# Kernel optimization log

Hardware: AMD Instinct MI355X
Metric: run time of the kernel (lower is better)

The kernel has to match this reference:

```python
import jax, jax.numpy as jnp
import numpy as np

DIM = 192
HEADS = 4
B, H, W = 4, 128, 128


def _dwconv3(x, w):
    # depthwise 3x3, padding=1: w has shape [C, 1, 3, 3], groups = C
    return jax.lax.conv_general_dilated(
        x, w, window_strides=(1, 1), padding='SAME',
        feature_group_count=x.shape[1],
        dimension_numbers=('NCHW', 'OIHW', 'NCHW'))


def _conv1x1(x, w):
    # w: [O, C] (squeezed 1x1 kernel), bias=False
    return jnp.einsum('bchw,oc->bohw', x, w)


def _l2norm(t):
    # torch F.normalize(dim=-1), eps=1e-12
    n = jnp.sqrt(jnp.sum(t * t, axis=-1, keepdims=True))
    return t / jnp.maximum(n, 1e-12)


def setup_inputs() -> dict:
    key = jax.random.key(0)
    ks = jax.random.split(key, 12)
    s = 0.05
    return {
        'x': jax.random.normal(ks[0], (B, DIM, H, W), jnp.float32),
        'x_hidden': jax.random.normal(ks[1], (B, DIM, H, W), jnp.float32),
        'qkv_w': jax.random.normal(ks[2], (3 * DIM, DIM), jnp.float32) * s,
        'qkv_dw_w': jax.random.normal(ks[3], (3 * DIM, 1, 3, 3), jnp.float32) * s,
        'q_mut_w': jax.random.normal(ks[4], (DIM, DIM), jnp.float32) * s,
        'q_mut_dw_w': jax.random.normal(ks[5], (DIM, 1, 3, 3), jnp.float32) * s,
        'kv_mut_w': jax.random.normal(ks[6], (2 * DIM, DIM), jnp.float32) * s,
        'kv_mut_dw_w': jax.random.normal(ks[7], (2 * DIM, 1, 3, 3), jnp.float32) * s,
        'proj_w': jax.random.normal(ks[8], (DIM, 2 * DIM), jnp.float32) * s,
        'temperature': jnp.ones((HEADS, 1, 1), jnp.float32),
        'temperature_mut': jnp.ones((HEADS, 1, 1), jnp.float32),
    }


def reference(x, x_hidden, qkv_w, qkv_dw_w, q_mut_w, q_mut_dw_w,
              kv_mut_w, kv_mut_dw_w, proj_w, temperature, temperature_mut):
    b, c, h, w = x.shape
    heads = HEADS

    qkv = _dwconv3(_conv1x1(x, qkv_w), qkv_dw_w)
    q, k, v = jnp.split(qkv, 3, axis=1)
    q_mut = _dwconv3(_conv1x1(x, q_mut_w), q_mut_dw_w)
    kv_mut = _dwconv3(_conv1x1(x_hidden, kv_mut_w), kv_mut_dw_w)
    k_mut, v_mut = jnp.split(kv_mut, 2, axis=1)

    def rs(t):  # b (head c') h w -> b head c' (h w)
        return t.reshape(b, heads, c // heads, h * w)

    q, k, v = rs(q), rs(k), rs(v)
    q_mut, k_mut, v_mut = rs(q_mut), rs(k_mut), rs(v_mut)

    q, k = _l2norm(q), _l2norm(k)
    q_mut, k_mut = _l2norm(q_mut), _l2norm(k_mut)

    # channel-wise (transposed) attention: [b, head, c', c']
    attn = jax.nn.softmax(
        jnp.einsum('bhcn,bhdn->bhcd', q, k) * temperature, axis=-1)
    cross = jax.nn.softmax(
        jnp.einsum('bhcn,bhdn->bhcd', q_mut, k_mut) * temperature_mut, axis=-1)

    out = jnp.einsum('bhcd,bhdn->bhcn', attn, v).reshape(b, c, h, w)
    out_mut = jnp.einsum('bhcd,bhdn->bhcn', cross, v_mut).reshape(b, c, h, w)

    return _conv1x1(jnp.concatenate((out, out_mut), axis=1), proj_w)
```

## Files before the change

kernel.cpp:

```cpp
#include <hip/hip_runtime.h>
#include <hip/hip_bf16.h>

typedef __hip_bfloat16 bf16;
using short8  = __attribute__((ext_vector_type(8))) short;
using float4_ = __attribute__((ext_vector_type(4))) float;

#define B_    4
#define C_    192
#define NN    16384
#define HEADS 4
#define CHD   48
#define TOT   1152

__device__ __forceinline__ float b2f(bf16 v) { return __bfloat162float(v); }
__device__ __forceinline__ float s2f(short s) {
    return __uint_as_float(((unsigned)(unsigned short)s) << 16);
}

__global__ __launch_bounds__(256) void kprep_w(
    const float* __restrict__ qkv_w, const float* __restrict__ qm_w,
    const float* __restrict__ kvm_w, bf16* __restrict__ Wb)
{
    int i = blockIdx.x * 256 + threadIdx.x;
    if (i >= TOT * C_) return;
    int r = i / C_, c = i % C_;
    float v = (r < 576) ? qkv_w[r * C_ + c]
            : (r < 768) ? qm_w[(r - 576) * C_ + c]
                        : kvm_w[(r - 768) * C_ + c];
    Wb[i] = __float2bfloat16(v);
}

__global__ __launch_bounds__(256) void kprep_x(
    const float* __restrict__ x, const float* __restrict__ xh,
    int b, bf16* __restrict__ Xt)
{
    const int src = blockIdx.z;
    const float* in = (src == 0 ? x : xh) + (size_t)b * C_ * NN;
    bf16* outp = Xt + (size_t)src * NN * C_;
    const int n0 = blockIdx.x * 32, c0 = blockIdx.y * 32;
    __shared__ float t[32][33];
    const int tid = threadIdx.x;
    const int ln = tid & 31, lc = tid >> 5;
    #pragma unroll
    for (int it = 0; it < 4; ++it)
        t[lc + it * 8][ln] = in[(size_t)(c0 + lc + it * 8) * NN + n0 + ln];
    __syncthreads();
    const int lc2 = tid & 31, ln2 = tid >> 5;
    #pragma unroll
    for (int it = 0; it < 4; ++it)
        outp[(size_t)(n0 + ln2 + it * 8) * C_ + c0 + lc2] =
            __float2bfloat16(t[lc2][ln2 + it * 8]);
}

__global__ __launch_bounds__(256) void kgemm(
    const bf16* __restrict__ Wb, const bf16* __restrict__ Xt,
    bf16* __restrict__ Y)
{
    const int nt0 = blockIdx.x * 128;
    const int mt0 = blockIdx.y * 64;
    const int tid = threadIdx.x;
    const bf16* Xs = Xt + (mt0 >= 768 ? (size_t)NN * C_ : 0);

    __shared__ short sA[64][72];
    __shared__ short sB[128][72];

    const int wave = tid >> 6, lane = tid & 63;
    const int mw = (wave & 1) * 32, nw = (wave >> 1) * 64;
    const int lm = lane & 15, lq = lane >> 4;

    float4_ acc[2][4];
    #pragma unroll
    for (int i = 0; i < 2; ++i)
        #pragma unroll
        for (int j = 0; j < 4; ++j)
            acc[i][j] = (float4_){0.f, 0.f, 0.f, 0.f};

    for (int kc = 0; kc < 192; kc += 64) {
        __syncthreads();
        {
            int r = tid >> 3, c8 = (tid & 7) * 8;
            #pragma unroll
            for (int it = 0; it < 2; ++it, r += 32)
                *(short8*)&sA[r][c8] =
                    *(const short8*)&Wb[(size_t)(mt0 + r) * C_ + kc + c8];
        }
        {
            int r = tid >> 3, c8 = (tid & 7) * 8;
            #pragma unroll
            for (int it = 0; it < 4; ++it, r += 32)
                *(short8*)&sB[r][c8] =
                    *(const short8*)&Xs[(size_t)(nt0 + r) * C_ + kc + c8];
        }
        __syncthreads();
        #pragma unroll
        for (int kk = 0; kk < 64; kk += 32) {
            short8 af[2], bfr[4];
            const int ko = kk + lq * 8;
            #pragma unroll
            for (int i = 0; i < 2; ++i)
                af[i] = *(const short8*)&sA[mw + i * 16 + lm][ko];
            #pragma unroll
            for (int j = 0; j < 4; ++j)
                bfr[j] = *(const short8*)&sB[nw + j * 16 + lm][ko];
            #pragma unroll
            for (int i = 0; i < 2; ++i)
                #pragma unroll
                for (int j = 0; j < 4; ++j)
                    acc[i][j] = __builtin_amdgcn_mfma_f32_16x16x32_bf16(
                        af[i], bfr[j], acc[i][j], 0, 0, 0);
        }
    }
    #pragma unroll
    for (int i = 0; i < 2; ++i)
        #pragma unroll
        for (int j = 0; j < 4; ++j) {
            const int n = nt0 + nw + j * 16 + lm;
            #pragma unroll
            for (int r = 0; r < 4; ++r) {
                const int m = mt0 + mw + i * 16 + lq * 4 + r;
                Y[(size_t)m * NN + n] = __float2bfloat16(acc[i][j][r]);
            }
        }
}

__device__ __forceinline__ void kdw_load_row(
    float* r, const bf16* __restrict__ Yc, int row, int x0, int lane)
{
    float f[8];
    if (row >= 0 && row <= 127) {
        short8 v = *(const short8*)(Yc + row * 128 + x0);
        #pragma unroll
        for (int i = 0; i < 8; ++i) f[i] = s2f(v[i]);
    } else {
        #pragma unroll
        for (int i = 0; i < 8; ++i) f[i] = 0.f;
    }
    const float lf = __shfl(f[7], lane - 1);
    const float rf = __shfl(f[0], lane + 1);
    r[0] = (x0 > 0)   ? lf : 0.f;
    r[9] = (x0 < 120) ? rf : 0.f;
    #pragma unroll
    for (int i = 0; i < 8; ++i) r[i + 1] = f[i];
}

__global__ __launch_bounds__(256) void kdw(
    const bf16* __restrict__ Y,
    const float* __restrict__ qkv_dw, const float* __restrict__ qm_dw,
    const float* __restrict__ kvm_dw, int b, bf16* __restrict__ QT,
    float* __restrict__ nrmsq)
{
    const int ch  = blockIdx.x;
    const int tid = threadIdx.x;
    const int tx = tid & 15, ty = tid >> 4;
    const int lane = tid & 63;
    const int x0 = tx * 8;
    const int y0 = blockIdx.y * 64 + ty * 4;

    const float* dwp = (ch < 576) ? qkv_dw + (size_t)ch * 9
                     : (ch < 768) ? qm_dw + (size_t)(ch - 576) * 9
                                  : kvm_dw + (size_t)(ch - 768) * 9;
    float w[9];
    #pragma unroll
    for (int i = 0; i < 9; ++i) w[i] = dwp[i];

    const bf16* Yc = Y + (size_t)ch * NN;
    bf16* qout = QT + ((size_t)b * TOT + ch) * NN;

    float r0[10], r1[10], r2[10];
    kdw_load_row(r0, Yc, y0 - 1, x0, lane);
    kdw_load_row(r1, Yc, y0,     x0, lane);

    float ssq = 0.f;
    #pragma unroll
    for (int yy = 0; yy < 4; ++yy) {
        kdw_load_row(r2, Yc, y0 + yy + 1, x0, lane);
        short8 sv;
        #pragma unroll
        for (int xx = 0; xx < 8; ++xx) {
            float s = w[0] * r0[xx] + w[1] * r0[xx + 1] + w[2] * r0[xx + 2]
                    + w[3] * r1[xx] + w[4] * r1[xx + 1] + w[5] * r1[xx + 2]
                    + w[6] * r2[xx] + w[7] * r2[xx + 1] + w[8] * r2[xx + 2];
            ssq += s * s;
            bf16 h = __float2bfloat16(s);
            sv[xx] = *reinterpret_cast<short*>(&h);
        }
        *(short8*)&qout[(size_t)(y0 + yy) * 128 + x0] = sv;
        #pragma unroll
        for (int i = 0; i < 10; ++i) { r0[i] = r1[i]; r1[i] = r2[i]; }
    }

    int cls = -1, ci = 0;
    if (ch < 192)                    { cls = 0; ci = ch; }
    else if (ch < 384)               { cls = 1; ci = ch - 192; }
    else if (ch >= 576 && ch < 768)  { cls = 2; ci = ch - 576; }
    else if (ch >= 768 && ch < 960)  { cls = 3; ci = ch - 768; }
    if (cls >= 0) {
        #pragma unroll
        for (int off = 32; off > 0; off >>= 1) ssq += __shfl_down(ssq, off);
        __shared__ float red[4];
        if ((tid & 63) == 0) red[tid >> 6] = ssq;
        __syncthreads();
        if (tid == 0)
            atomicAdd(&nrmsq[(b * 4 + cls) * 192 + ci],
                      red[0] + red[1] + red[2] + red[3]);
    }
}

__global__ __launch_bounds__(256) void k3_mfma(
    const bf16* __restrict__ QT, float* __restrict__ Gpart)
{
    const int chunk = blockIdx.x;
    const int t = blockIdx.y >> 2, h = blockIdx.y & 3;
    const int b = blockIdx.z;
    const int qch = (t == 0 ? 0 : 576) + h * CHD;
    const int kch = (t == 0 ? 192 : 768) + h * CHD;
    const bf16* qp = QT + ((size_t)b * TOT + qch) * NN;
    const bf16* kp = QT + ((size_t)b * TOT + kch) * NN;

    const int tid = threadIdx.x;
    const int wave = tid >> 6, lane = tid & 63;
    const int lm = lane & 15, lq = lane >> 4;
    const int n0 = chunk * 512 + wave * 128;

    float4_ acc[3][3];
    #pragma unroll
    for (int i = 0; i < 3; ++i)
        #pragma unroll
        for (int j = 0; j < 3; ++j)
            acc[i][j] = (float4_){0.f, 0.f, 0.f, 0.f};

    #pragma unroll
    for (int kk = 0; kk < 128; kk += 32) {
        short8 af[3], bfr[3];
        const int ko = n0 + kk + lq * 8;
        #pragma unroll
        for (int i = 0; i < 3; ++i)
            af[i] = *(const short8*)&qp[(size_t)(i * 16 + lm) * NN + ko];
        #pragma unroll
        for (int j = 0; j < 3; ++j)
            bfr[j] = *(const short8*)&kp[(size_t)(j * 16 + lm) * NN + ko];
        #pragma unroll
        for (int i = 0; i < 3; ++i)
            #pragma unroll
            for (int j = 0; j < 3; ++j)
                acc[i][j] = __builtin_amdgcn_mfma_f32_16x16x32_bf16(
                    af[i], bfr[j], acc[i][j], 0, 0, 0);
    }

    __shared__ float sW[4][48 * 49];
    #pragma unroll
    for (int i = 0; i < 3; ++i)
        #pragma unroll
        for (int j = 0; j < 3; ++j)
            #pragma unroll
            for (int r = 0; r < 4; ++r)
                sW[wave][(i * 16 + lq * 4 + r) * 49 + j * 16 + lm] = acc[i][j][r];
    __syncthreads();

    const int gidx = ((t * 4 + b) * 4 + h);
    float* Gp = Gpart + ((size_t)gidx * 32 + chunk) * 2304;
    for (int idx = tid; idx < 2304; idx += 256) {
        const int c = idx / 48, d = idx % 48;
        Gp[idx] = sW[0][c * 49 + d] + sW[1][c * 49 + d]
                + sW[2][c * 49 + d] + sW[3][c * 49 + d];
    }
}

__global__ __launch_bounds__(256) void kred(
    const float* __restrict__ Gpart, float* __restrict__ G)
{
    const int idx = blockIdx.x * 256 + threadIdx.x;
    if (idx >= 32 * 2304) return;
    const int g = idx / 2304, i = idx % 2304;
    const float* p = Gpart + (size_t)g * 32 * 2304 + i;
    float s = 0.f;
    #pragma unroll
    for (int ch = 0; ch < 32; ++ch) s += p[(size_t)ch * 2304];
    G[(size_t)g * 2304 + i] = s;
}

__global__ __launch_bounds__(256) void k4a_softmax(
    const float* __restrict__ G, const float* __restrict__ nrmsq,
    const float* __restrict__ tq, const float* __restrict__ tm,
    float* __restrict__ P)
{
    const int gidx = blockIdx.x;
    const int h = gidx & 3, tb = gidx >> 2;
    const int b = tb & 3, t = tb >> 2;
    const float* Gp = G + (size_t)gidx * 2304;
    float* Pp = P + (size_t)gidx * 2304;

    const int tid = threadIdx.x;
    const int wave = tid >> 6, lane = tid & 63;
    const int clsq = (t == 0) ? 0 : 2, clsk = (t == 0) ? 1 : 3;
    const float tmp = (t == 0 ? tq[h] : tm[h]);

    float nk = 1.f;
    if (lane < 48)
        nk = fmaxf(sqrtf(fmaxf(nrmsq[(b * 4 + clsk) * 192 + h * 48 + lane], 0.f)),
                   1e-12f);
    const float sk = tmp / nk;

    const int c0 = blockIdx.y * 12 + wave * 3;
    #pragma unroll
    for (int cc = 0; cc < 3; ++cc) {
        const int c = c0 + cc;
        const float nq =
            fmaxf(sqrtf(fmaxf(nrmsq[(b * 4 + clsq) * 192 + h * 48 + c], 0.f)),
                  1e-12f);
        float L = -1e30f;
        if (lane < 48) L = Gp[c * 48 + lane] * sk / nq;
        float mx = L;
        #pragma unroll
        for (int off = 32; off > 0; off >>= 1)
            mx = fmaxf(mx, __shfl_xor(mx, off));
        float e = (lane < 48) ? expf(L - mx) : 0.f;
        float sum = e;
        #pragma unroll
        for (int off = 32; off > 0; off >>= 1)
            sum += __shfl_xor(sum, off);
        if (lane < 48) Pp[c * 48 + lane] = e / sum;
    }
}

__global__ __launch_bounds__(256) void k4b_fold(
    const float* __restrict__ P, const float* __restrict__ proj_w,
    bf16* __restrict__ Mb)
{
    const int gidx = blockIdx.x;
    const int h = gidx & 3, tb = gidx >> 2;
    const int b = tb & 3, t = tb >> 2;
    const int o0 = blockIdx.y * 48;
    const int colb = t * 192 + h * 48;

    __shared__ float sP[48][49];
    __shared__ float sW[48][49];
    const int tid = threadIdx.x;
    const float* Pp = P + (size_t)gidx * 2304;

    for (int idx = tid; idx < 2304; idx += 256) {
        const int r = idx / 48, q = idx % 48;
        sP[r][q] = Pp[idx];
        sW[r][q] = proj_w[(size_t)(o0 + r) * 384 + colb + q];
    }
    __syncthreads();

    for (int idx = tid; idx < 2304; idx += 256) {
        const int o = idx / 48, d = idx % 48;
        float s = 0.f;
        #pragma unroll
        for (int c = 0; c < 48; ++c) s += sW[o][c] * sP[c][d];
        Mb[((size_t)b * 192 + o0 + o) * 384 + colb + d] = __float2bfloat16(s);
    }
}

__global__ __launch_bounds__(512, 4) void k5_mfma(
    const bf16* __restrict__ Mb, const bf16* __restrict__ QT,
    float* __restrict__ out)
{
    const int nt0 = blockIdx.x * 128;
    const int b   = blockIdx.z;
    const int tid = threadIdx.x;

    __shared__ short sM[192][72];
    __shared__ short sB[128][72];

    const int wave = tid >> 6, lane = tid & 63;
    const int wm = (wave >> 2) * 96;
    const int wn = (wave & 3) * 32;
    const int lm = lane & 15, lq = lane >> 4;

    const bf16* Qb = QT + (size_t)b * TOT * NN;
    const bf16* Mp = Mb + (size_t)b * 192 * 384;

    float4_ acc[6][2];
    #pragma unroll
    for (int i = 0; i < 6; ++i)
        #pragma unroll
        for (int j = 0; j < 2; ++j)
            acc[i][j] = (float4_){0.f, 0.f, 0.f, 0.f};

    for (int kc = 0; kc < 384; kc += 64) {
        __syncthreads();
        #pragma unroll
        for (int it = 0; it < 3; ++it) {
            const int id = it * 512 + tid;
            const int r = id >> 3, g = (id & 7) * 8;
            *(short8*)&sM[r][g] =
                *(const short8*)&Mp[(size_t)r * 384 + kc + g];
        }
        const int chbase = (kc < 192) ? (384 + kc) : (960 + (kc - 192));
        #pragma unroll
        for (int it = 0; it < 2; ++it) {
            const int t = it * 512 + tid;
            const int d = t & 63, ng = t >> 6;
            short8 v = *(const short8*)
                &Qb[(size_t)(chbase + d) * NN + nt0 + ng * 8];
            #pragma unroll
            for (int j = 0; j < 8; ++j)
                sB[ng * 8 + j][d] = v[j];
        }
        __syncthreads();
        #pragma unroll
        for (int kk = 0; kk < 64; kk += 32) {
            short8 af[6], bfr[2];
            const int ko = kk + lq * 8;
            #pragma unroll
            for (int i = 0; i < 6; ++i)
                af[i] = *(const short8*)&sM[wm + i * 16 + lm][ko];
            #pragma unroll
            for (int j = 0; j < 2; ++j)
                bfr[j] = *(const short8*)&sB[wn + j * 16 + lm][ko];
            #pragma unroll
            for (int i = 0; i < 6; ++i)
                #pragma unroll
                for (int j = 0; j < 2; ++j)
                    acc[i][j] = __builtin_amdgcn_mfma_f32_16x16x32_bf16(
                        af[i], bfr[j], acc[i][j], 0, 0, 0);
        }
    }
    #pragma unroll
    for (int i = 0; i < 6; ++i)
        #pragma unroll
        for (int j = 0; j < 2; ++j) {
            const int n = nt0 + wn + j * 16 + lm;
            #pragma unroll
            for (int r = 0; r < 4; ++r) {
                const int m = wm + i * 16 + lq * 4 + r;
                out[((size_t)b * C_ + m) * NN + n] = acc[i][j][r];
            }
        }
}

extern "C" void kernel_launch(void* const* d_in, const int* in_sizes, int n_in,
                              void* d_out, int out_size, void* d_ws, size_t ws_size,
                              hipStream_t stream)
{
    const float* x     = (const float*)d_in[0];
    const float* xh    = (const float*)d_in[1];
    const float* qkvw  = (const float*)d_in[2];
    const float* qkvdw = (const float*)d_in[3];
    const float* qmw   = (const float*)d_in[4];
    const float* qmdw  = (const float*)d_in[5];
    const float* kvmw  = (const float*)d_in[6];
    const float* kvmdw = (const float*)d_in[7];
    const float* projw = (const float*)d_in[8];
    const float* tq    = (const float*)d_in[9];
    const float* tm    = (const float*)d_in[10];
    float* out = (float*)d_out;

    char* ws = (char*)d_ws;
    size_t off = 0;
    bf16*  QT = (bf16*)(ws + off);  off += (size_t)B_ * TOT * NN * 2;
    bf16*  Y  = (bf16*)(ws + off);  off += (size_t)TOT * NN * 2;
    bf16*  Xt = (bf16*)(ws + off);  off += (size_t)2 * NN * C_ * 2;
    bf16*  Wb = (bf16*)(ws + off);  off += (size_t)TOT * C_ * 2;
    float* nrm = (float*)(ws + off); off += (size_t)B_ * 4 * 192 * 4;
    float* G   = (float*)(ws + off); off += (size_t)2 * B_ * HEADS * 48 * 48 * 4;
    bf16*  Mb  = (bf16*)(ws + off);  off += (size_t)B_ * 192 * 384 * 2;
    float* Gpart = (float*)(ws + off); off += (size_t)32 * 32 * 2304 * 4;
    float* P = Gpart;

    hipMemsetAsync(nrm, 0, (size_t)B_ * 4 * 192 * 4, stream);

    kprep_w<<<dim3((TOT * C_ + 255) / 256), 256, 0, stream>>>(qkvw, qmw, kvmw, Wb);

    for (int b = 0; b < B_; ++b) {
        kprep_x<<<dim3(512, 6, 2), 256, 0, stream>>>(x, xh, b, Xt);
        kgemm  <<<dim3(128, 18), 256, 0, stream>>>(Wb, Xt, Y);
        kdw    <<<dim3(1152, 2), 256, 0, stream>>>(Y, qkvdw, qmdw, kvmdw, b, QT, nrm);
    }

    k3_mfma    <<<dim3(32, 8, B_), 256, 0, stream>>>(QT, Gpart);
    kred       <<<dim3((32 * 2304 + 255) / 256), 256, 0, stream>>>(Gpart, G);
    k4a_softmax<<<dim3(32, 4), 256, 0, stream>>>(G, nrm, tq, tm, P);
    k4b_fold   <<<dim3(32, 4), 256, 0, stream>>>(P, projw, Mb);
    k5_mfma    <<<dim3(128, 1, B_), 512, 0, stream>>>(Mb, QT, out);
}
```

Measured before the change: 359.5 us.

## Enlarge GEMM M-tile to 128 and vectorize transpose kernel with 64x64 tiles

The 1x1-conv GEMM now uses 128x128 block tiles with each wave computing a 64x64 sub-tile (4x4 MFMA accumulators), halving the number of blocks and reloading the X tile fewer times per output. The input transpose kernel moves to 64x64 tiles with float4 global loads and 8-wide bf16 vector stores, replacing scalar accesses. The larger tile raises register and LDS use per block, which may lower occupancy. The boundary check mt0>=768 still holds because 768 is a multiple of 128.

```diff
diff --git a/kernel.cpp b/kernel.cpp
--- a/kernel.cpp
+++ b/kernel.cpp
@@ -37,19 +37,32 @@
     const int src = blockIdx.z;
     const float* in = (src == 0 ? x : xh) + (size_t)b * C_ * NN;
     bf16* outp = Xt + (size_t)src * NN * C_;
-    const int n0 = blockIdx.x * 32, c0 = blockIdx.y * 32;
-    __shared__ float t[32][33];
-    const int tid = threadIdx.x;
-    const int ln = tid & 31, lc = tid >> 5;
-    #pragma unroll
-    for (int it = 0; it < 4; ++it)
-        t[lc + it * 8][ln] = in[(size_t)(c0 + lc + it * 8) * NN + n0 + ln];
+    const int n0 = blockIdx.x * 64, c0 = blockIdx.y * 64;
+    __shared__ float t[64][65];
+    const int tid = threadIdx.x;
+
+    #pragma unroll
+    for (int it = 0; it < 4; ++it) {
+        const int id = it * 256 + tid;
+        const int c = id >> 4, i4 = (id & 15) * 4;
+        const float4_ v = *(const float4_*)&in[(size_t)(c0 + c) * NN + n0 + i4];
+        t[c][i4 + 0] = v[0]; t[c][i4 + 1] = v[1];
+        t[c][i4 + 2] = v[2]; t[c][i4 + 3] = v[3];
+    }
     __syncthreads();
-    const int lc2 = tid & 31, ln2 = tid >> 5;
-    #pragma unroll
-    for (int it = 0; it < 4; ++it)
-        outp[(size_t)(n0 + ln2 + it * 8) * C_ + c0 + lc2] =
-            __float2bfloat16(t[lc2][ln2 + it * 8]);
+
+    #pragma unroll
+    for (int it = 0; it < 2; ++it) {
+        const int id = it * 256 + tid;
+        const int n = id >> 3, j8 = (id & 7) * 8;
+        short8 sv;
+        #pragma unroll
+        for (int k = 0; k < 8; ++k) {
+            bf16 h = __float2bfloat16(t[j8 + k][n]);
+            sv[k] = *reinterpret_cast<short*>(&h);
+        }
+        *(short8*)&outp[(size_t)(n0 + n) * C_ + c0 + j8] = sv;
+    }
 }
 
 __global__ __launch_bounds__(256) void kgemm(
@@ -57,20 +70,20 @@
     bf16* __restrict__ Y)
 {
     const int nt0 = blockIdx.x * 128;
-    const int mt0 = blockIdx.y * 64;
+    const int mt0 = blockIdx.y * 128;
     const int tid = threadIdx.x;
     const bf16* Xs = Xt + (mt0 >= 768 ? (size_t)NN * C_ : 0);
 
-    __shared__ short sA[64][72];
+    __shared__ short sA[128][72];
     __shared__ short sB[128][72];
 
     const int wave = tid >> 6, lane = tid & 63;
-    const int mw = (wave & 1) * 32, nw = (wave >> 1) * 64;
+    const int wm = (wave & 1) * 64, wn = (wave >> 1) * 64;
     const int lm = lane & 15, lq = lane >> 4;
 
-    float4_ acc[2][4];
-    #pragma unroll
-    for (int i = 0; i < 2; ++i)
+    float4_ acc[4][4];
+    #pragma unroll
+    for (int i = 0; i < 4; ++i)
         #pragma unroll
         for (int j = 0; j < 4; ++j)
             acc[i][j] = (float4_){0.f, 0.f, 0.f, 0.f};
@@ -80,30 +93,26 @@
         {
             int r = tid >> 3, c8 = (tid & 7) * 8;
             #pragma unroll
-            for (int it = 0; it < 2; ++it, r += 32)
+            for (int it = 0; it < 4; ++it, r += 32) {
                 *(short8*)&sA[r][c8] =
                     *(const short8*)&Wb[(size_t)(mt0 + r) * C_ + kc + c8];
-        }
-        {
-            int r = tid >> 3, c8 = (tid & 7) * 8;
-            #pragma unroll
-            for (int it = 0; it < 4; ++it, r += 32)
                 *(short8*)&sB[r][c8] =
                     *(const short8*)&Xs[(size_t)(nt0 + r) * C_ + kc + c8];
+            }
         }
         __syncthreads();
         #pragma unroll
         for (int kk = 0; kk < 64; kk += 32) {
-            short8 af[2], bfr[4];
+            short8 af[4], bfr[4];
             const int ko = kk + lq * 8;
             #pragma unroll
-            for (int i = 0; i < 2; ++i)
-                af[i] = *(const short8*)&sA[mw + i * 16 + lm][ko];
+            for (int i = 0; i < 4; ++i)
+                af[i] = *(const short8*)&sA[wm + i * 16 + lm][ko];
             #pragma unroll
             for (int j = 0; j < 4; ++j)
-                bfr[j] = *(const short8*)&sB[nw + j * 16 + lm][ko];
-            #pragma unroll
-            for (int i = 0; i < 2; ++i)
+                bfr[j] = *(const short8*)&sB[wn + j * 16 + lm][ko];
+            #pragma unroll
+            for (int i = 0; i < 4; ++i)
                 #pragma unroll
                 for (int j = 0; j < 4; ++j)
                     acc[i][j] = __builtin_amdgcn_mfma_f32_16x16x32_bf16(
@@ -111,13 +120,13 @@
         }
     }
     #pragma unroll
-    for (int i = 0; i < 2; ++i)
+    for (int i = 0; i < 4; ++i)
         #pragma unroll
         for (int j = 0; j < 4; ++j) {
-            const int n = nt0 + nw + j * 16 + lm;
+            const int n = nt0 + wn + j * 16 + lm;
             #pragma unroll
             for (int r = 0; r < 4; ++r) {
-                const int m = mt0 + mw + i * 16 + lq * 4 + r;
+                const int m = mt0 + wm + i * 16 + lq * 4 + r;
                 Y[(size_t)m * NN + n] = __float2bfloat16(acc[i][j][r]);
             }
         }
@@ -466,8 +475,8 @@
     kprep_w<<<dim3((TOT * C_ + 255) / 256), 256, 0, stream>>>(qkvw, qmw, kvmw, Wb);
 
     for (int b = 0; b < B_; ++b) {
-        kprep_x<<<dim3(512, 6, 2), 256, 0, stream>>>(x, xh, b, Xt);
-        kgemm  <<<dim3(128, 18), 256, 0, stream>>>(Wb, Xt, Y);
+        kprep_x<<<dim3(256, 3, 2), 256, 0, stream>>>(x, xh, b, Xt);
+        kgemm  <<<dim3(128, 9), 256, 0, stream>>>(Wb, Xt, Y);
         kdw    <<<dim3(1152, 2), 256, 0, stream>>>(Y, qkvdw, qmdw, kvmdw, b, QT, nrm);
     }
 
```

Measured after the change: 385.5 us. +7.2%, slower.
